# Performance work log

Hardware: AMD Instinct MI355X
Metric: run time of the kernel (lower is better)

## Reference

```python
import jax, jax.numpy as jnp
import numpy as np

TOPK = 1024
C = 32
FC0 = 256
EPS_BN = 1e-5
EPS_NORM = 1e-12


def setup_inputs() -> dict:
    key = jax.random.key(0)
    ks = jax.random.split(key, 8)
    B, L = 128, 16384
    N = B * L
    x = jax.random.normal(ks[0], (N, C), dtype=jnp.float32)
    length = jnp.full((B,), L, dtype=jnp.int32)
    # conv1d_1: Conv1d(32, 1, 1) -> weight [1, 32, 1] ~ vector [32], bias [1]
    w_att = jax.random.normal(ks[1], (C,), dtype=jnp.float32) * (1.0 / np.sqrt(C))
    b_att = jnp.zeros((1,), dtype=jnp.float32)
    # bn_1: BatchNorm1d(1) (eval mode: use running stats)
    g1 = jnp.ones((1,), dtype=jnp.float32)
    be1 = jnp.zeros((1,), dtype=jnp.float32)
    rm1 = jnp.zeros((1,), dtype=jnp.float32)
    rv1 = jnp.ones((1,), dtype=jnp.float32)
    # fc_1: Linear(TOPK*C, FC0)
    fan_in = TOPK * C
    W_fc = jax.random.normal(ks[2], (FC0, fan_in), dtype=jnp.float32) * (1.0 / np.sqrt(fan_in))
    b_fc = jnp.zeros((FC0,), dtype=jnp.float32)
    # bn_2: BatchNorm1d(FC0) (eval mode)
    g2 = jnp.ones((FC0,), dtype=jnp.float32)
    be2 = jnp.zeros((FC0,), dtype=jnp.float32)
    rm2 = jnp.zeros((FC0,), dtype=jnp.float32)
    rv2 = jnp.ones((FC0,), dtype=jnp.float32)
    return {"x": x, "length": length, "w_att": w_att, "b_att": b_att,
            "g1": g1, "be1": be1, "rm1": rm1, "rv1": rv1,
            "W_fc": W_fc, "b_fc": b_fc,
            "g2": g2, "be2": be2, "rm2": rm2, "rv2": rv2}


def reference(x, length, w_att, b_att, g1, be1, rm1, rv1, W_fc, b_fc, g2, be2, rm2, rv2):
    B = length.shape[0]
    N = x.shape[0]
    L = N // B  # equal-length segments (sum(length) == N)
    # attention score: 1x1 conv over channels + BatchNorm1d(1) (eval)
    att = x @ w_att + b_att[0]                                   # [N]
    att = (att - rm1[0]) * (g1[0] / jnp.sqrt(rv1[0] + EPS_BN)) + be1[0]
    # per-segment descending sort + take top TOPK == top_k per segment
    att_b = att.reshape(B, L)                                    # [B, L]
    x_b = x.reshape(B, L, C)                                     # [B, L, C]
    _, idx = jax.lax.top_k(att_b, TOPK)                          # [B, TOPK]
    ranked = jnp.take_along_axis(x_b, idx[:, :, None], axis=1)   # [B, TOPK, C]
    flat = ranked.reshape(B, TOPK * C)                           # [B, TOPK*C]
    # fc_1 + bn_2 (eval) + L2 row-normalize
    out = flat @ W_fc.T + b_fc                                   # [B, FC0]
    out = (out - rm2) * (g2 / jnp.sqrt(rv2 + EPS_BN)) + be2
    nrm = jnp.maximum(jnp.linalg.norm(out, axis=1, keepdims=True), EPS_NORM)
    return out / nrm
```

## Files before the change

### kernel.cpp

```cpp
#include <hip/hip_runtime.h>
#include <stdint.h>

#define CC 32
#define TOPK 1024
#define FC0 256
#define HL 8192

__device__ __forceinline__ uint64_t cex(uint64_t v, int s, bool up, int t)
{
    uint64_t o = (uint64_t)__shfl_xor((unsigned long long)v, s, 64);
    bool left = ((t & s) == 0);
    uint64_t mn = v < o ? v : o;
    uint64_t mx = v < o ? o : v;
    return (left == up) ? mn : mx;
}

__global__ __launch_bounds__(1024)
void k_seltop(const float* __restrict__ x,
              const float* __restrict__ w_att, const float* __restrict__ b_att,
              uint64_t* __restrict__ cand)
{
    __shared__ float tile[512][CC + 1];
    __shared__ uint32_t kv[HL];
    __shared__ uint64_t cv[2048];
    __shared__ uint32_t hist[257];
    __shared__ uint32_t s_prefix, s_k, s_cnt;
    const int t = threadIdx.x;
    const int b = blockIdx.x;
    const int lane = t & 63;
    const uint32_t halfbase = (uint32_t)(b & 1) * HL;

    if (t == 0) { s_prefix = 0; s_k = TOPK; s_cnt = 0; }

    for (int c = 0; c < 16; ++c) {
        const size_t rowbase = (size_t)b * HL + (size_t)c * 512;
        const float4* xv = (const float4*)(x + rowbase * CC);
        __syncthreads();
        #pragma unroll
        for (int i = 0; i < 4; ++i) {
            int e = i * 1024 + t;
            float4 v = xv[e];
            int r = e >> 3, c4 = (e & 7) * 4;
            tile[r][c4 + 0] = v.x; tile[r][c4 + 1] = v.y;
            tile[r][c4 + 2] = v.z; tile[r][c4 + 3] = v.w;
        }
        __syncthreads();
        if (t < 512) {
            float p[8];
            #pragma unroll
            for (int j = 0; j < 8; ++j) {
                float pj = __fmul_rn(tile[t][j], w_att[j]);
                pj = __fmaf_rn(tile[t][8 + j],  w_att[8 + j],  pj);
                pj = __fmaf_rn(tile[t][16 + j], w_att[16 + j], pj);
                pj = __fmaf_rn(tile[t][24 + j], w_att[24 + j], pj);
                p[j] = pj;
            }
            float q0 = __fadd_rn(p[0], p[1]);
            float q1 = __fadd_rn(p[2], p[3]);
            float q2 = __fadd_rn(p[4], p[5]);
            float q3 = __fadd_rn(p[6], p[7]);
            float dot = __fadd_rn(__fadd_rn(q0, q1), __fadd_rn(q2, q3));
            float v = __fadd_rn(dot, b_att[0]);
            uint32_t bits = __float_as_uint(v);
            kv[c * 512 + t] = (bits & 0x80000000u) ? ~bits : (bits | 0x80000000u);
        }
    }
    __syncthreads();

    #pragma unroll
    for (int round = 0; round < 2; ++round) {
        if (t < 257) hist[t] = 0;
        __syncthreads();
        const uint32_t pref = s_prefix;
        const uint32_t k = s_k;
        for (int i = t; i < HL; i += 1024) {
            uint32_t u = kv[i];
            if (round == 0) atomicAdd(&hist[u >> 24], 1u);
            else if ((u >> 24) == pref) atomicAdd(&hist[(u >> 16) & 255u], 1u);
        }
        __syncthreads();
        if (t < 64) {
            int l = t;
            uint32_t h0 = hist[4*l], h1 = hist[4*l+1], h2 = hist[4*l+2], h3 = hist[4*l+3];
            uint32_t s3 = h3, s2 = h2 + s3, s1 = h1 + s2, s0 = h0 + s1;
            uint32_t tot = s0, run = tot;
            #pragma unroll
            for (int off = 1; off < 64; off <<= 1) {
                int src = l + off < 64 ? l + off : 63;
                uint32_t o = __shfl(run, src, 64);
                if (l + off < 64) run += o;
            }
            uint32_t esuf = run - tot;
            hist[4*l]   = s0 + esuf; hist[4*l+1] = s1 + esuf;
            hist[4*l+2] = s2 + esuf; hist[4*l+3] = s3 + esuf;
        }
        __syncthreads();
        if (t < 256) {
            uint32_t st = hist[t], sn = hist[t + 1];
            if (st >= k && sn < k) {
                s_prefix = (pref << 8) | (uint32_t)t;
                s_k = k - sn;
            }
        }
        __syncthreads();
    }
    const uint32_t T = s_prefix << 16;

    for (int i = t; i < HL; i += 1024) {
        bool q = kv[i] >= T;
        unsigned long long m = __ballot(q);
        uint32_t base = 0;
        if (lane == 0 && m)
            base = atomicAdd(&s_cnt, (uint32_t)__popcll(m));
        base = __shfl(base, 0);
        if (q) {
            uint32_t pos = base + (uint32_t)__popcll(m & ((1ULL << lane) - 1ULL));
            if (pos < 2048)
                cv[pos] = ((uint64_t)kv[i] << 32)
                        | (uint64_t)(uint32_t)(~(halfbase + (uint32_t)i));
        }
    }
    __syncthreads();
    const uint32_t mm = s_cnt < 2048u ? s_cnt : 2048u;
    for (int i = t; i < 2048; i += 1024)
        if ((uint32_t)i >= mm) cv[i] = 0ULL;
    __syncthreads();

    {
        uint64_t r0 = cv[t], r1 = cv[t + 1024];
        #pragma unroll
        for (int size = 2; size <= 64; size <<= 1) {
            bool up = ((t & size) == 0);
            #pragma unroll
            for (int s = size >> 1; s > 0; s >>= 1) {
                r0 = cex(r0, s, up, t);
                r1 = cex(r1, s, up, t);
            }
        }
        cv[t] = r0; cv[t + 1024] = r1;
    }
    #pragma unroll
    for (int size = 128; size <= 2048; size <<= 1) {
        for (int s = size >> 1; s >= 64; s >>= 1) {
            __syncthreads();
            int i = ((t & ~(s - 1)) << 1) | (t & (s - 1));
            int j = i | s;
            uint64_t va = cv[i], vb = cv[j];
            bool up = ((i & size) == 0);
            if (up ? (va > vb) : (va < vb)) { cv[i] = vb; cv[j] = va; }
        }
        __syncthreads();
        {
            uint64_t a0 = cv[t], a1 = cv[t + 1024];
            bool up0, up1;
            if (size <= 512)      { up0 = ((t & size) == 0); up1 = up0; }
            else if (size == 1024){ up0 = true;  up1 = false; }
            else                  { up0 = true;  up1 = true;  }
            #pragma unroll
            for (int s = 32; s > 0; s >>= 1) {
                a0 = cex(a0, s, up0, t);
                a1 = cex(a1, s, up1, t);
            }
            cv[t] = a0; cv[t + 1024] = a1;
        }
        __syncthreads();
    }
    cand[(size_t)b * TOPK + t] = cv[2047 - t];
}

__global__ __launch_bounds__(1024)
void k_merge(const uint64_t* __restrict__ cand, int* __restrict__ idx_out)
{
    __shared__ uint64_t cv[2048];
    const int t = threadIdx.x;
    const int seg = blockIdx.x;
    cv[t]        = cand[(size_t)(seg * 2) * TOPK + t];
    cv[1024 + t] = cand[(size_t)(seg * 2 + 1) * TOPK + (1023 - t)];
    __syncthreads();
    for (int s = 1024; s >= 1; s >>= 1) {
        int i = ((t & ~(s - 1)) << 1) | (t & (s - 1));
        int j = i | s;
        uint64_t va = cv[i], vb = cv[j];
        if (va < vb) { cv[i] = vb; cv[j] = va; }
        __syncthreads();
    }
    idx_out[(size_t)seg * TOPK + t] = (int)(~(uint32_t)cv[t]);
}

#define FT 64
#define KCI 32
#define NKC 128
#define KCHUNK 256

__global__ __launch_bounds__(256)
void k_fc(const float* __restrict__ x, const int* __restrict__ idx,
          const float* __restrict__ W, float* __restrict__ part, int L)
{
    __shared__ float flT[KCI][128];
    __shared__ float wT[KCI][FT];
    const int t = threadIdx.x;
    const int kc = blockIdx.x;
    const int fb = blockIdx.y * FT;
    const int tb = t >> 4, tf = t & 15;
    float acc[8][4];
    #pragma unroll
    for (int i = 0; i < 8; ++i)
        #pragma unroll
        for (int j = 0; j < 4; ++j) acc[i][j] = 0.f;

    const int b_ld = t >> 1, half = t & 1;
    for (int sub = 0; sub < KCHUNK / KCI; ++sub) {
        const int kbase = kc * KCHUNK + sub * KCI;
        const int t_idx = kbase >> 5;
        {
            int row = idx[b_ld * TOPK + t_idx];
            row = row < 0 ? 0 : (row >= L ? L - 1 : row);
            const float* src = x + ((size_t)b_ld * L + row) * CC + half * 16;
            #pragma unroll
            for (int q = 0; q < 4; ++q) {
                float4 v = ((const float4*)src)[q];
                int c0 = half * 16 + q * 4;
                flT[c0 + 0][b_ld] = v.x; flT[c0 + 1][b_ld] = v.y;
                flT[c0 + 2][b_ld] = v.z; flT[c0 + 3][b_ld] = v.w;
            }
        }
        {
            #pragma unroll
            for (int i2 = 0; i2 < 2; ++i2) {
                int e = t + i2 * 256;
                int fl = e >> 3, u = e & 7;
                const float4 v = *(const float4*)(W + (size_t)(fb + fl) * (TOPK * CC) + kbase + u * 4);
                wT[u * 4 + 0][fl] = v.x; wT[u * 4 + 1][fl] = v.y;
                wT[u * 4 + 2][fl] = v.z; wT[u * 4 + 3][fl] = v.w;
            }
        }
        __syncthreads();
        #pragma unroll
        for (int kk = 0; kk < KCI; ++kk) {
            float bb[8], ww[4];
            *(float4*)&bb[0] = *(const float4*)&flT[kk][tb * 8];
            *(float4*)&bb[4] = *(const float4*)&flT[kk][tb * 8 + 4];
            *(float4*)&ww[0] = *(const float4*)&wT[kk][tf * 4];
            #pragma unroll
            for (int i = 0; i < 8; ++i)
                #pragma unroll
                for (int j = 0; j < 4; ++j)
                    acc[i][j] = fmaf(bb[i], ww[j], acc[i][j]);
        }
        __syncthreads();
    }
    float* pbase = part + ((size_t)kc * 128) * 256 + fb + tf * 4;
    #pragma unroll
    for (int i = 0; i < 8; ++i) {
        float* dst = pbase + (size_t)(tb * 8 + i) * 256;
        ((float4*)dst)[0] = make_float4(acc[i][0], acc[i][1], acc[i][2], acc[i][3]);
    }
}

__global__ __launch_bounds__(256)
void k_post(const float* __restrict__ part, const float* __restrict__ b_fc,
            const float* __restrict__ g2, const float* __restrict__ be2,
            const float* __restrict__ rm2, const float* __restrict__ rv2,
            float* __restrict__ out)
{
    __shared__ float red[256];
    const int b = blockIdx.x, f = threadIdx.x;
    float s = 0.f;
    #pragma unroll 8
    for (int kc = 0; kc < NKC; ++kc)
        s += part[((size_t)kc * 128 + b) * 256 + f];
    s += b_fc[f];
    float o = (s - rm2[f]) * (g2[f] / sqrtf(rv2[f] + 1e-5f)) + be2[f];
    red[f] = o * o;
    __syncthreads();
    for (int st = 128; st > 0; st >>= 1) {
        if (f < st) red[f] += red[f + st];
        __syncthreads();
    }
    float nrm = fmaxf(sqrtf(red[0]), 1e-12f);
    out[(size_t)b * 256 + f] = o / nrm;
}

extern "C" void kernel_launch(void* const* d_in, const int* in_sizes, int n_in,
                              void* d_out, int out_size, void* d_ws, size_t ws_size,
                              hipStream_t stream)
{
    const float* x     = (const float*)d_in[0];
    const float* w_att = (const float*)d_in[2];
    const float* b_att = (const float*)d_in[3];
    const float* W_fc  = (const float*)d_in[8];
    const float* b_fc  = (const float*)d_in[9];
    const float* g2    = (const float*)d_in[10];
    const float* be2   = (const float*)d_in[11];
    const float* rm2   = (const float*)d_in[12];
    const float* rv2   = (const float*)d_in[13];

    const int N = in_sizes[0] / CC;
    const int B = in_sizes[1];
    const int L = N / B;

    uint8_t* ws = (uint8_t*)d_ws;
    uint64_t* cand = (uint64_t*)(ws);
    int* idx       = (int*)(ws + (size_t)2 * B * TOPK * 8);
    float* part    = (float*)(ws + (size_t)2 * B * TOPK * 8 + (size_t)B * TOPK * 4);

    k_seltop<<<2 * B, 1024, 0, stream>>>(x, w_att, b_att, cand);
    k_merge<<<B, 1024, 0, stream>>>(cand, idx);
    dim3 g3(NKC, FC0 / FT);
    k_fc<<<g3, 256, 0, stream>>>(x, idx, W_fc, part, L);
    k_post<<<B, 256, 0, stream>>>(part, b_fc, g2, be2, rm2, rv2, (float*)d_out);
}
```

Before: 115.4 us.

## Split attention scoring into a separate high-parallelism kernel before half selection

Moves the per-row attention dot product and key encoding out of the 1024-thread selection kernel into its own kernel with many small 256-thread blocks, which writes the sortable keys to a workspace buffer. The selection kernel then just loads the precomputed keys into shared memory. The aim is to stream x at higher occupancy and better bandwidth than the 256 large blocks, which used only half their threads during scoring. The cost is an extra launch plus a global write and read of the keys (N*4 bytes) and more workspace.

Result: no change. 115.2 us (median of 2 runs) (-0.2%).

```diff
diff --git a/kernel.cpp b/kernel.cpp
--- a/kernel.cpp
+++ b/kernel.cpp
@@ -15,12 +15,46 @@
     return (left == up) ? mn : mx;
 }
 
+__global__ __launch_bounds__(256)
+void k_att(const float* __restrict__ x,
+           const float* __restrict__ w_att, const float* __restrict__ b_att,
+           uint32_t* __restrict__ key, int N)
+{
+    __shared__ float tile[256][CC + 1];
+    const int t = threadIdx.x;
+    const size_t base = (size_t)blockIdx.x * 256;
+    const float4* xv = (const float4*)(x + base * CC);
+    #pragma unroll
+    for (int i = 0; i < 8; ++i) {
+        int e = i * 256 + t;
+        float4 v = xv[e];
+        int r = e >> 3, c4 = (e & 7) * 4;
+        tile[r][c4 + 0] = v.x; tile[r][c4 + 1] = v.y;
+        tile[r][c4 + 2] = v.z; tile[r][c4 + 3] = v.w;
+    }
+    __syncthreads();
+    float p[8];
+    #pragma unroll
+    for (int j = 0; j < 8; ++j) {
+        float pj = __fmul_rn(tile[t][j], w_att[j]);
+        pj = __fmaf_rn(tile[t][8 + j],  w_att[8 + j],  pj);
+        pj = __fmaf_rn(tile[t][16 + j], w_att[16 + j], pj);
+        pj = __fmaf_rn(tile[t][24 + j], w_att[24 + j], pj);
+        p[j] = pj;
+    }
+    float q0 = __fadd_rn(p[0], p[1]);
+    float q1 = __fadd_rn(p[2], p[3]);
+    float q2 = __fadd_rn(p[4], p[5]);
+    float q3 = __fadd_rn(p[6], p[7]);
+    float dot = __fadd_rn(__fadd_rn(q0, q1), __fadd_rn(q2, q3));
+    float v = __fadd_rn(dot, b_att[0]);
+    uint32_t bits = __float_as_uint(v);
+    key[base + t] = (bits & 0x80000000u) ? ~bits : (bits | 0x80000000u);
+}
+
 __global__ __launch_bounds__(1024)
-void k_seltop(const float* __restrict__ x,
-              const float* __restrict__ w_att, const float* __restrict__ b_att,
-              uint64_t* __restrict__ cand)
-{
-    __shared__ float tile[512][CC + 1];
+void k_halfsel(const uint32_t* __restrict__ key, uint64_t* __restrict__ cand)
+{
     __shared__ uint32_t kv[HL];
     __shared__ uint64_t cv[2048];
     __shared__ uint32_t hist[257];
@@ -30,41 +64,13 @@
     const int lane = t & 63;
     const uint32_t halfbase = (uint32_t)(b & 1) * HL;
 
+    {
+        const uint4* ks = (const uint4*)(key + (size_t)b * HL);
+        uint4 a = ks[t], c = ks[t + 1024];
+        *(uint4*)&kv[t * 4] = a;
+        *(uint4*)&kv[(t + 1024) * 4] = c;
+    }
     if (t == 0) { s_prefix = 0; s_k = TOPK; s_cnt = 0; }
-
-    for (int c = 0; c < 16; ++c) {
-        const size_t rowbase = (size_t)b * HL + (size_t)c * 512;
-        const float4* xv = (const float4*)(x + rowbase * CC);
-        __syncthreads();
-        #pragma unroll
-        for (int i = 0; i < 4; ++i) {
-            int e = i * 1024 + t;
-            float4 v = xv[e];
-            int r = e >> 3, c4 = (e & 7) * 4;
-            tile[r][c4 + 0] = v.x; tile[r][c4 + 1] = v.y;
-            tile[r][c4 + 2] = v.z; tile[r][c4 + 3] = v.w;
-        }
-        __syncthreads();
-        if (t < 512) {
-            float p[8];
-            #pragma unroll
-            for (int j = 0; j < 8; ++j) {
-                float pj = __fmul_rn(tile[t][j], w_att[j]);
-                pj = __fmaf_rn(tile[t][8 + j],  w_att[8 + j],  pj);
-                pj = __fmaf_rn(tile[t][16 + j], w_att[16 + j], pj);
-                pj = __fmaf_rn(tile[t][24 + j], w_att[24 + j], pj);
-                p[j] = pj;
-            }
-            float q0 = __fadd_rn(p[0], p[1]);
-            float q1 = __fadd_rn(p[2], p[3]);
-            float q2 = __fadd_rn(p[4], p[5]);
-            float q3 = __fadd_rn(p[6], p[7]);
-            float dot = __fadd_rn(__fadd_rn(q0, q1), __fadd_rn(q2, q3));
-            float v = __fadd_rn(dot, b_att[0]);
-            uint32_t bits = __float_as_uint(v);
-            kv[c * 512 + t] = (bits & 0x80000000u) ? ~bits : (bits | 0x80000000u);
-        }
-    }
     __syncthreads();
 
     #pragma unroll
@@ -299,12 +305,19 @@
     const int B = in_sizes[1];
     const int L = N / B;
 
+    const size_t off_key  = 0;
+    const size_t off_cand = off_key + (size_t)N * 4;
+    const size_t off_idx  = off_cand + (size_t)2 * B * TOPK * 8;
+    const size_t off_part = off_idx + (size_t)B * TOPK * 4;
+
     uint8_t* ws = (uint8_t*)d_ws;
-    uint64_t* cand = (uint64_t*)(ws);
-    int* idx       = (int*)(ws + (size_t)2 * B * TOPK * 8);
-    float* part    = (float*)(ws + (size_t)2 * B * TOPK * 8 + (size_t)B * TOPK * 4);
-
-    k_seltop<<<2 * B, 1024, 0, stream>>>(x, w_att, b_att, cand);
+    uint32_t* key  = (uint32_t*)(ws + off_key);
+    uint64_t* cand = (uint64_t*)(ws + off_cand);
+    int* idx       = (int*)(ws + off_idx);
+    float* part    = (float*)(ws + off_part);
+
+    k_att<<<N / 256, 256, 0, stream>>>(x, w_att, b_att, key, N);
+    k_halfsel<<<2 * B, 1024, 0, stream>>>(key, cand);
     k_merge<<<B, 1024, 0, stream>>>(cand, idx);
     dim3 g3(NKC, FC0 / FT);
     k_fc<<<g3, 256, 0, stream>>>(x, idx, W_fc, part, L);
```
